# Kernel tuning notes

Hardware: AMD Instinct MI355X
Metric: run time of the kernel (lower is better)

Reference implementation:

```python
import jax, jax.numpy as jnp
import numpy as np

B, N, H, W = 4, 16, 480, 640
Hf, Wf, C = 120, 160, 128
NUM_CLASSES = 14
NUM_EXPERTS = NUM_CLASSES - 1  # 13 per-class ROI experts
ROI = 14  # ROI-align output resolution


def setup_inputs() -> dict:
    key = jax.random.key(0)
    ks = jax.random.split(key, 20)
    inp = {
        'depth': jax.random.normal(ks[0], (B, 1, H, W), jnp.float32),
        'context': jax.random.normal(ks[1], (B, 192, Hf, Wf), jnp.float32),
        'input_feature_map': jax.random.normal(ks[2], (B, C, Hf, Wf), jnp.float32),
        'bin_num': 64,
        'min_depth': 1,
        'max_depth': 10,
        'masks': jax.random.uniform(ks[3], (B, N, Hf, Wf), jnp.float32),
        'instances': jax.random.uniform(ks[4], (B, N, H, W), jnp.float32),
        'boxes': jax.random.uniform(ks[5], (B, N, 4), jnp.float32),
        'labels': jax.random.randint(ks[6], (B, N), 0, NUM_EXPERTS),
    }
    s = 0.05
    # per-class (expert) parameters, stacked on leading expert axis
    inp['w_conv_s'] = s * jax.random.normal(ks[7], (NUM_EXPERTS, C, C, 3, 3), jnp.float32)
    inp['b_conv_s'] = jnp.zeros((NUM_EXPERTS, C), jnp.float32)
    inp['w_fc'] = s * jax.random.normal(ks[8], (NUM_EXPERTS, 2, C), jnp.float32)
    inp['b_fc'] = jnp.zeros((NUM_EXPERTS, 2), jnp.float32)
    inp['w_conv_c1'] = s * jax.random.normal(ks[9], (NUM_EXPERTS, 64, C, 3, 3), jnp.float32)
    inp['b_conv_c1'] = jnp.zeros((NUM_EXPERTS, 64), jnp.float32)
    inp['w_conv_c2'] = s * jax.random.normal(ks[10], (NUM_EXPERTS, 1, 64, 3, 3), jnp.float32)
    inp['b_conv_c2'] = jnp.zeros((NUM_EXPERTS, 1), jnp.float32)
    return inp


def _boxes_norm(boxes_flat):
    # map raw rand [M,4] -> valid normalized (y1,x1,y2,x2) in [0,1]
    y1 = 0.6 * boxes_flat[:, 0]
    x1 = 0.6 * boxes_flat[:, 1]
    y2 = y1 + 0.1 + 0.3 * boxes_flat[:, 2]
    x2 = x1 + 0.1 + 0.3 * boxes_flat[:, 3]
    return y1, x1, y2, x2


def _roi_align(fmap, batch_idx, boxes_flat, R):
    # fmap [B,C,Hf,Wf] -> [M,C,R,R] bilinear ROI sampling (irregular gather)
    _, _, hf, wf = fmap.shape
    y1, x1, y2, x2 = _boxes_norm(boxes_flat)
    t = (jnp.arange(R, dtype=fmap.dtype) + 0.5) / R
    ys = (y1[:, None] + (y2 - y1)[:, None] * t) * (hf - 1)  # [M,R]
    xs = (x1[:, None] + (x2 - x1)[:, None] * t) * (wf - 1)
    y0 = jnp.clip(jnp.floor(ys).astype(jnp.int32), 0, hf - 2)
    x0 = jnp.clip(jnp.floor(xs).astype(jnp.int32), 0, wf - 2)
    wy = jnp.clip(ys - y0, 0.0, 1.0)[:, :, None, None]   # [M,R,1,1]
    wx = jnp.clip(xs - x0, 0.0, 1.0)[:, None, :, None]   # [M,1,R,1]
    b = batch_idx[:, None, None]
    Y0 = y0[:, :, None]
    X0 = x0[:, None, :]
    def g(dy, dx):
        return fmap[b, :, Y0 + dy, X0 + dx]  # [M,R,R,C]
    out = (g(0, 0) * (1 - wy) * (1 - wx) + g(0, 1) * (1 - wy) * wx
           + g(1, 0) * wy * (1 - wx) + g(1, 1) * wy * wx)
    return jnp.transpose(out, (0, 3, 1, 2))  # [M,C,R,R]


def _conv(x, w, b):
    # x [Cin,R,R], w [Cout,Cin,3,3] -> [Cout,R,R]
    y = jax.lax.conv_general_dilated(x[None], w, (1, 1), 'SAME',
                                     dimension_numbers=('NCHW', 'OIHW', 'NCHW'))[0]
    return y + b[:, None, None]

_conv_v = jax.vmap(_conv)  # per-instance expert conv (per-instance weights)


def reference(depth, context, input_feature_map, bin_num, min_depth, max_depth,
              masks, instances, boxes, labels,
              w_conv_s, b_conv_s, w_fc, b_fc, w_conv_c1, b_conv_c1, w_conv_c2, b_conv_c2):
    b_, n_, h, w = instances.shape
    M = b_ * n_
    lab = labels.reshape(M)
    batch_idx = jnp.repeat(jnp.arange(b_), n_)
    boxes_flat = boxes.reshape(M, 4)

    # shared ROI gather of class-routed instances
    roi = _roi_align(input_feature_map, batch_idx, boxes_flat, ROI)  # [M,C,R,R]

    # hard routing: gather each instance's class-expert weights by label
    hs = jax.nn.relu(_conv_v(roi, w_conv_s[lab], b_conv_s[lab]))     # [M,C,R,R]
    gap = hs.mean(axis=(2, 3))                                        # [M,C]
    ss = jnp.einsum('mc,moc->mo', gap, w_fc[lab]) + b_fc[lab]         # [M,2]
    scale = ss[:, 0].reshape(b_, n_)
    shift = ss[:, 1].reshape(b_, n_)

    h1 = jax.nn.relu(_conv_v(roi, w_conv_c1[lab], b_conv_c1[lab]))    # [M,64,R,R]
    c = _conv_v(h1, w_conv_c2[lab], b_conv_c2[lab])                   # [M,1,R,R]
    canonical = jax.image.resize(c, (M, 1, h, w), method='bilinear')
    canonical = canonical.reshape(b_, n_, h, w)

    # loss_type == 0: relu(.).clamp(min=0.001) == max(., 0.001)
    depth_r = jnp.maximum(canonical * scale[..., None, None] + shift[..., None, None], 0.001)
    return depth_r, canonical, scale, shift
```

## Files before the change

### kernel.cpp

```cpp
#include <hip/hip_runtime.h>


typedef unsigned short bfu;
typedef __attribute__((ext_vector_type(8))) short bf16x8;
typedef __attribute__((ext_vector_type(4))) float f32x4;

__device__ __forceinline__ float bf2f(bfu u) {
  union { unsigned int i; float f; } v;
  v.i = ((unsigned int)u) << 16;
  return v.f;
}
__device__ __forceinline__ bfu f2bf(float f) {
  union { float f; unsigned int i; } v;
  v.f = f;
  unsigned int u = v.i;
  u = (u + 0x7fffu + ((u >> 16) & 1u)) >> 16;
  return (bfu)u;
}

#define B_  4
#define N_  16
#define M_  64
#define H_  480
#define W_  640
#define HF  120
#define WF  160
#define C_  128
#define R_  14
#define PIX 196
#define NE  13
#define KK  1152

#define WS_XB    0
#define WS_XH    802816
#define WS_C     1204224
#define WS_GAP   1216768
#define WS_SCALE 1224960
#define WS_SHIFT 1225024
#define WS_WF    1225088
#define WS_BIASF 2662784
#define WS_W2    2665280
#define WS_B2    2672768
#define WS_WFC   2672784
#define WS_BFC   2676112

#define XB_BLOCKS 256
#define PREP_BLOCKS 1024

__global__ __launch_bounds__(256) void prep_xb_kernel(
    const float* __restrict__ fmap, const float* __restrict__ boxes,
    const float* __restrict__ w_s, const float* __restrict__ b_s,
    const float* __restrict__ w_fc, const float* __restrict__ b_fc,
    const float* __restrict__ w_c1, const float* __restrict__ b_c1,
    const float* __restrict__ w_c2, const float* __restrict__ b_c2,
    float* __restrict__ ws)
{
  int tid = threadIdx.x;
  if (blockIdx.x < XB_BLOCKS) {
    __shared__ int iy0[R_], ix0[R_];
    __shared__ float swy[R_], swx[R_];
    __shared__ unsigned int lt[PIX][17];
    int m  = blockIdx.x >> 2;
    int cb = (blockIdx.x & 3) * 32;
    if (tid < 2*R_) {
      int r = tid % R_;
      bool isY = tid < R_;
      float b0 = boxes[m*4 + (isY ? 0 : 1)];
      float b2 = boxes[m*4 + (isY ? 2 : 3)];
      float lo = 0.6f * b0;
      float hi = lo + 0.1f + 0.3f * b2;
      float t = ((float)r + 0.5f) / (float)R_;
      float dim = isY ? (float)(HF-1) : (float)(WF-1);
      float s = (lo + (hi - lo) * t) * dim;
      int maxi = isY ? (HF-2) : (WF-2);
      int i0 = (int)floorf(s);
      i0 = i0 < 0 ? 0 : (i0 > maxi ? maxi : i0);
      float w = s - (float)i0;
      w = w < 0.f ? 0.f : (w > 1.f ? 1.f : w);
      if (isY) { iy0[r] = i0; swy[r] = w; } else { ix0[r] = i0; swx[r] = w; }
    }
    __syncthreads();
    int bi = m / N_;
    const float* fb = fmap + ((size_t)bi * C_ + cb) * HF * WF;
    if (tid < PIX) {
      int ry = tid / 14, rx = tid - (tid/14)*14;
      int y0 = iy0[ry], x0 = ix0[rx];
      float wy = swy[ry], wx = swx[rx];
      float w00 = (1.f-wy)*(1.f-wx), w01 = (1.f-wy)*wx;
      float w10 = wy*(1.f-wx),       w11 = wy*wx;
      const float* fp = fb + (size_t)y0*WF + x0;
      #pragma unroll 4
      for (int c2 = 0; c2 < 16; ++c2) {
        const float* f0 = fp + (size_t)(2*c2)*HF*WF;
        const float* f1 = f0 + (size_t)HF*WF;
        float v0 = f0[0]*w00 + f0[1]*w01 + f0[WF]*w10 + f0[WF+1]*w11;
        float v1 = f1[0]*w00 + f1[1]*w01 + f1[WF]*w10 + f1[WF+1]*w11;
        lt[tid][c2] = (unsigned int)f2bf(v0) | ((unsigned int)f2bf(v1) << 16);
      }
    }
    __syncthreads();
    unsigned int* xbw = (unsigned int*)(ws + WS_XB);
    for (int idx = tid; idx < PIX*16; idx += 256) {
      int p = idx >> 4, c2 = idx & 15;
      xbw[((size_t)m*PIX + p)*64 + (cb >> 1) + c2] = lt[p][c2];
    }
    return;
  }

  const int P0 = NE*192*KK;
  const int P1 = NE*192;
  const int P2 = NE*576;
  const int P3 = NE;
  const int P4 = NE*256;
  const int P5 = NE*2;
  const int P6 = M_*C_;
  int total = P0+P1+P2+P3+P4+P5+P6;
  bfu* wf = (bfu*)(ws + WS_WF);
  for (int idx = (blockIdx.x - XB_BLOCKS)*256 + tid; idx < total;
       idx += PREP_BLOCKS*256) {
    int d = idx;
    if (d < P0) {
      int e = d / (192*KK);
      int r = d - e*(192*KK);
      int oc = r / KK;
      int k  = r - oc*KK;
      int kidx = k >> 7, ic = k & 127;
      float v = (oc < 128) ? w_s[((e*128 + oc)*128 + ic)*9 + kidx]
                           : w_c1[((e*64 + (oc-128))*128 + ic)*9 + kidx];
      wf[d] = f2bf(v);
      continue;
    }
    d -= P0;
    if (d < P1) {
      int e = d / 192, oc = d - e*192;
      ws[WS_BIASF + d] = (oc < 128) ? b_s[e*128 + oc] : b_c1[e*64 + oc - 128];
      continue;
    }
    d -= P1;
    if (d < P2) {
      int e = d / 576, k = d - e*576;
      int kidx = k >> 6, ic = k & 63;
      ws[WS_W2 + d] = w_c2[(e*64 + ic)*9 + kidx];
      continue;
    }
    d -= P2;
    if (d < P3) { ws[WS_B2 + d] = b_c2[d]; continue; }
    d -= P3;
    if (d < P4) { ws[WS_WFC + d] = w_fc[d]; continue; }
    d -= P4;
    if (d < P5) { ws[WS_BFC + d] = b_fc[d]; continue; }
    d -= P5;
    ws[WS_GAP + d] = 0.f;
  }
}

__global__ __launch_bounds__(256) void gemm_kernel(
    const int* __restrict__ labels, float* __restrict__ ws)
{
  __shared__ bfu lA[128*32];
  __shared__ bfu lB[128*32];
  const bfu* Xb = (const bfu*)(ws + WS_XB);
  const bfu* WFp = (const bfu*)(ws + WS_WF);
  const float* biasf = ws + WS_BIASF;
  float* gap = ws + WS_GAP;
  bfu* Xh = (bfu*)(ws + WS_XH);

  int bx = blockIdx.x;
  int m  = bx >> 2;
  int mb = (bx >> 1) & 1;
  int nb = bx & 1;
  int e = labels[m];
  int tid = threadIdx.x;
  int wave = tid >> 6, lane = tid & 63;
  int wm = wave >> 1, wn = wave & 1;
  int l15 = lane & 15, q = lane >> 4;

  int row0 = tid >> 2, row1 = row0 + 64;
  int kc = tid & 3;
  int loff0 = row0*32 + (kc ^ ((row0 >> 1) & 3))*8;
  int loff1 = row1*32 + (kc ^ ((row1 >> 1) & 3))*8;
  int g0 = mb*128 + row0, g1 = mb*128 + row1;
  bool av0 = g0 < 192, av1 = g1 < 192;
  const bfu* wfe = WFp + (size_t)e*192*KK;
  const bfu* wr0 = wfe + (size_t)g0*KK + kc*8;
  const bfu* wr1 = wfe + (size_t)g1*KK + kc*8;
  int pg0 = nb*128 + row0, pg1 = nb*128 + row1;
  int py0 = pg0 / 14, px0 = pg0 - (pg0/14)*14;
  int py1 = pg1 / 14, px1 = pg1 - (pg1/14)*14;
  bool pv0 = pg0 < PIX, pv1 = pg1 < PIX;
  const bfu* xbm = Xb + (size_t)m*PIX*128;

  f32x4 acc[4][4];
  #pragma unroll
  for (int i = 0; i < 4; ++i)
    #pragma unroll
    for (int j = 0; j < 4; ++j)
      acc[i][j] = (f32x4){0.f, 0.f, 0.f, 0.f};

  const uint4 z4 = make_uint4(0,0,0,0);
  uint4 na0, na1, nb0, nb1;
  auto issue = [&](int s, uint4& A0, uint4& A1, uint4& B0, uint4& B1) {
    int kidx = s >> 2, icc = s & 3;
    int t3 = kidx / 3;
    int dy = t3 - 1, dx = (kidx - t3*3) - 1;
    A0 = av0 ? *(const uint4*)(wr0 + s*32) : z4;
    A1 = av1 ? *(const uint4*)(wr1 + s*32) : z4;
    int ys0 = py0 + dy, xs0 = px0 + dx;
    int ys1 = py1 + dy, xs1 = px1 + dx;
    bool v0 = pv0 && (unsigned)ys0 < 14u && (unsigned)xs0 < 14u;
    bool v1 = pv1 && (unsigned)ys1 < 14u && (unsigned)xs1 < 14u;
    B0 = v0 ? *(const uint4*)(xbm + (size_t)(ys0*14+xs0)*128 + icc*32 + kc*8) : z4;
    B1 = v1 ? *(const uint4*)(xbm + (size_t)(ys1*14+xs1)*128 + icc*32 + kc*8) : z4;
  };
  issue(0, na0, na1, nb0, nb1);

  for (int s = 0; s < 36; ++s) {
    __syncthreads();
    *(uint4*)&lA[loff0] = na0;
    *(uint4*)&lA[loff1] = na1;
    *(uint4*)&lB[loff0] = nb0;
    *(uint4*)&lB[loff1] = nb1;
    __syncthreads();
    if (s < 35) issue(s+1, na0, na1, nb0, nb1);
    bf16x8 af[4], bfr[4];
    #pragma unroll
    for (int i = 0; i < 4; ++i) {
      int r = wm*64 + i*16 + l15;
      af[i] = *(const bf16x8*)&lA[r*32 + (q ^ ((r >> 1) & 3))*8];
    }
    #pragma unroll
    for (int j = 0; j < 4; ++j) {
      int r = wn*64 + j*16 + l15;
      bfr[j] = *(const bf16x8*)&lB[r*32 + (q ^ ((r >> 1) & 3))*8];
    }
    #pragma unroll
    for (int i = 0; i < 4; ++i)
      #pragma unroll
      for (int j = 0; j < 4; ++j)
        acc[i][j] = __builtin_amdgcn_mfma_f32_16x16x32_bf16(af[i], bfr[j], acc[i][j], 0, 0, 0);
  }

  if (mb == 0) {
    #pragma unroll
    for (int i = 0; i < 4; ++i) {
      int ocb = wm*64 + i*16 + q*4;
      f32x4 bv = *(const f32x4*)&biasf[e*192 + ocb];
      #pragma unroll
      for (int r = 0; r < 4; ++r) {
        float sum = 0.f;
        #pragma unroll
        for (int j = 0; j < 4; ++j) {
          int p = nb*128 + wn*64 + j*16 + l15;
          float v = acc[i][j][r] + bv[r];
          v = v > 0.f ? v : 0.f;
          if (p < PIX) sum += v;
        }
        sum += __shfl_xor(sum, 1);
        sum += __shfl_xor(sum, 2);
        sum += __shfl_xor(sum, 4);
        sum += __shfl_xor(sum, 8);
        if (l15 == 0) atomicAdd(&gap[m*C_ + ocb + r], sum);
      }
    }
  } else if (wm == 0) {
    #pragma unroll
    for (int i = 0; i < 4; ++i) {
      int icb = i*16 + q*4;
      f32x4 bv = *(const f32x4*)&biasf[e*192 + 128 + icb];
      #pragma unroll
      for (int j = 0; j < 4; ++j) {
        int p = nb*128 + wn*64 + j*16 + l15;
        if (p < PIX) {
          ushort4 pk;
          float v0 = acc[i][j][0] + bv[0]; v0 = v0 > 0.f ? v0 : 0.f;
          float v1 = acc[i][j][1] + bv[1]; v1 = v1 > 0.f ? v1 : 0.f;
          float v2 = acc[i][j][2] + bv[2]; v2 = v2 > 0.f ? v2 : 0.f;
          float v3 = acc[i][j][3] + bv[3]; v3 = v3 > 0.f ? v3 : 0.f;
          pk.x = f2bf(v0); pk.y = f2bf(v1); pk.z = f2bf(v2); pk.w = f2bf(v3);
          *(ushort4*)&Xh[((size_t)m*PIX + p)*64 + icb] = pk;
        }
      }
    }
  }
}

__global__ __launch_bounds__(256) void convc2_kernel(
    const int* __restrict__ labels, float* __restrict__ ws,
    float* __restrict__ out)
{
  __shared__ bfu xh[PIX*64];
  __shared__ float w2l[576];
  int m = blockIdx.x;
  int e = labels[m];
  int tid = threadIdx.x;
  int wave = tid >> 6, lane = tid & 63;

  if (wave < 2) {
    const float* g  = ws + WS_GAP + m*C_;
    const float* wv = ws + WS_WFC + (e*2 + wave)*C_;
    float s = g[lane]*wv[lane] + g[lane+64]*wv[lane+64];
    #pragma unroll
    for (int d = 32; d; d >>= 1) s += __shfl_xor(s, d);
    if (lane == 0) {
      s = ws[WS_BFC + e*2 + wave] + s * (1.f/(float)PIX);
      size_t base = (size_t)2 * M_ * H_ * W_;
      if (wave == 0) { ws[WS_SCALE + m] = s; out[base + m] = s; }
      else           { ws[WS_SHIFT + m] = s; out[base + M_ + m] = s; }
    }
  }

  const bfu* Xh = (const bfu*)(ws + WS_XH) + (size_t)m*PIX*64;
  for (int i = tid; i < PIX*64/8; i += 256)
    *(uint4*)&xh[i*8] = *(const uint4*)&Xh[i*8];
  for (int i = tid; i < 576; i += 256)
    w2l[i] = ws[WS_W2 + e*576 + i];
  __syncthreads();
  if (tid < PIX) {
    int y = tid / 14, x = tid - (tid/14)*14;
    float acc = 0.f;
    #pragma unroll
    for (int kidx = 0; kidx < 9; ++kidx) {
      int ys = y + kidx/3 - 1, xs = x + (kidx - (kidx/3)*3) - 1;
      if ((unsigned)ys < 14u && (unsigned)xs < 14u) {
        const bfu* xr = xh + (ys*14 + xs)*64;
        const float* wr = w2l + kidx*64;
        #pragma unroll
        for (int cc = 0; cc < 8; ++cc) {
          bf16x8 xv = *(const bf16x8*)&xr[cc*8];
          f32x4 wa = *(const f32x4*)&wr[cc*8];
          f32x4 wb = *(const f32x4*)&wr[cc*8 + 4];
          acc += bf2f((bfu)xv[0])*wa[0] + bf2f((bfu)xv[1])*wa[1]
               + bf2f((bfu)xv[2])*wa[2] + bf2f((bfu)xv[3])*wa[3]
               + bf2f((bfu)xv[4])*wb[0] + bf2f((bfu)xv[5])*wb[1]
               + bf2f((bfu)xv[6])*wb[2] + bf2f((bfu)xv[7])*wb[3];
        }
      }
    }
    ws[WS_C + m*PIX + tid] = acc + ws[WS_B2 + e];
  }
}

__global__ __launch_bounds__(256) void resize_kernel(
    const float* __restrict__ ws_c, const float* __restrict__ ws_scale,
    const float* __restrict__ ws_shift, float* __restrict__ out)
{
  __shared__ float cs[PIX];
  int bx = blockIdx.x;
  int m = bx / 150;
  int chunk = bx % 150;
  int tid = threadIdx.x;
  if (tid < PIX) cs[tid] = ws_c[m*PIX + tid];
  __syncthreads();
  float sc = ws_scale[m], sh = ws_shift[m];
  int q0 = chunk*2048 + tid*8;
  int y = q0 / W_;
  int x0i = q0 - y*W_;
  float py = ((float)y + 0.5f) * (14.f/(float)H_) - 0.5f;
  py = fminf(fmaxf(py, 0.f), 13.f);
  int y0 = (int)py; y0 = y0 > 12 ? 12 : y0;
  float wy = py - (float)y0;
  const float* r0 = cs + y0*R_;
  const float* r1 = r0 + R_;
  float vd[8], vc[8];
  #pragma unroll
  for (int u = 0; u < 8; ++u) {
    int x = x0i + u;
    float px = ((float)x + 0.5f) * (14.f/(float)W_) - 0.5f;
    px = fminf(fmaxf(px, 0.f), 13.f);
    int xq = (int)px; xq = xq > 12 ? 12 : xq;
    float wx = px - (float)xq;
    float v = (r0[xq]*(1.f-wx) + r0[xq+1]*wx) * (1.f-wy)
            + (r1[xq]*(1.f-wx) + r1[xq+1]*wx) * wy;
    vc[u] = v;
    vd[u] = fmaxf(v*sc + sh, 0.001f);
  }
  size_t base = (size_t)m * H_ * W_ + q0;
  float* od = out + base;
  float* oc = out + (size_t)M_*H_*W_ + base;
  f32x4 d0 = (f32x4){vd[0], vd[1], vd[2], vd[3]};
  f32x4 d1 = (f32x4){vd[4], vd[5], vd[6], vd[7]};
  f32x4 c0 = (f32x4){vc[0], vc[1], vc[2], vc[3]};
  f32x4 c1 = (f32x4){vc[4], vc[5], vc[6], vc[7]};
  __builtin_nontemporal_store(d0, (f32x4*)(od));
  __builtin_nontemporal_store(d1, (f32x4*)(od + 4));
  __builtin_nontemporal_store(c0, (f32x4*)(oc));
  __builtin_nontemporal_store(c1, (f32x4*)(oc + 4));
}

extern "C" void kernel_launch(void* const* d_in, const int* in_sizes, int n_in,
                              void* d_out, int out_size, void* d_ws, size_t ws_size,
                              hipStream_t stream) {
  const float* fmap  = (const float*)d_in[2];
  const float* boxes = (const float*)d_in[8];
  const int* labels  = (const int*)d_in[9];
  const float* w_s  = (const float*)d_in[10];
  const float* b_s  = (const float*)d_in[11];
  const float* w_fc = (const float*)d_in[12];
  const float* b_fc = (const float*)d_in[13];
  const float* w_c1 = (const float*)d_in[14];
  const float* b_c1 = (const float*)d_in[15];
  const float* w_c2 = (const float*)d_in[16];
  const float* b_c2 = (const float*)d_in[17];
  float* ws = (float*)d_ws;
  float* out = (float*)d_out;

  hipLaunchKernelGGL(prep_xb_kernel, dim3(XB_BLOCKS + PREP_BLOCKS), dim3(256), 0, stream,
                     fmap, boxes, w_s, b_s, w_fc, b_fc, w_c1, b_c1, w_c2, b_c2, ws);
  hipLaunchKernelGGL(gemm_kernel, dim3(M_*4), dim3(256), 0, stream,
                     labels, ws);
  hipLaunchKernelGGL(convc2_kernel, dim3(M_), dim3(256), 0, stream,
                     labels, ws, out);
  hipLaunchKernelGGL(resize_kernel, dim3(M_*150), dim3(256), 0, stream,
                     ws + WS_C, ws + WS_SCALE, ws + WS_SHIFT, out);
}
```

Baseline: 376.2 us.

## Fuse conv_c2 and FC head into GEMM kernel with full-pixel tiles

The GEMM kernel now covers all 196 pixels per block (2 blocks per instance instead of 4), so the GAP reduction and the 64-channel hidden activation stay entirely within one block. The FC scale/shift head and the conv_c2 3x3 convolution then run in that block using shared memory, which removes the separate convc2 kernel launch, the global Xh round trip, and the GAP atomics along with their zeroing. In exchange there are fewer blocks (128), more accumulator registers per thread (26 MFMA tiles), and the conv_c2 tail runs serially after the GEMM inside the block.

```diff
diff --git a/kernel.cpp b/kernel.cpp
--- a/kernel.cpp
+++ b/kernel.cpp
@@ -32,9 +32,7 @@
 #define KK  1152
 
 #define WS_XB    0
-#define WS_XH    802816
 #define WS_C     1204224
-#define WS_GAP   1216768
 #define WS_SCALE 1224960
 #define WS_SHIFT 1225024
 #define WS_WF    1225088
@@ -113,8 +111,7 @@
   const int P3 = NE;
   const int P4 = NE*256;
   const int P5 = NE*2;
-  const int P6 = M_*C_;
-  int total = P0+P1+P2+P3+P4+P5+P6;
+  int total = P0+P1+P2+P3+P4+P5;
   bfu* wf = (bfu*)(ws + WS_WF);
   for (int idx = (blockIdx.x - XB_BLOCKS)*256 + tid; idx < total;
        idx += PREP_BLOCKS*256) {
@@ -148,110 +145,114 @@
     d -= P3;
     if (d < P4) { ws[WS_WFC + d] = w_fc[d]; continue; }
     d -= P4;
-    if (d < P5) { ws[WS_BFC + d] = b_fc[d]; continue; }
-    d -= P5;
-    ws[WS_GAP + d] = 0.f;
+    if (d < P5) { ws[WS_BFC + d] = b_fc[d]; }
   }
 }
 
 __global__ __launch_bounds__(256) void gemm_kernel(
-    const int* __restrict__ labels, float* __restrict__ ws)
+    const int* __restrict__ labels, float* __restrict__ ws,
+    float* __restrict__ out)
 {
-  __shared__ bfu lA[128*32];
-  __shared__ bfu lB[128*32];
-  const bfu* Xb = (const bfu*)(ws + WS_XB);
+  __shared__ __align__(16) char smem[28672];
+  bfu* lA = (bfu*)smem;
+  bfu* lB = (bfu*)(smem + 8192);
+
+  const bfu* Xb  = (const bfu*)(ws + WS_XB);
   const bfu* WFp = (const bfu*)(ws + WS_WF);
   const float* biasf = ws + WS_BIASF;
-  float* gap = ws + WS_GAP;
-  bfu* Xh = (bfu*)(ws + WS_XH);
 
   int bx = blockIdx.x;
-  int m  = bx >> 2;
-  int mb = (bx >> 1) & 1;
-  int nb = bx & 1;
+  int m  = bx >> 1;
+  int mb = bx & 1;
   int e = labels[m];
   int tid = threadIdx.x;
   int wave = tid >> 6, lane = tid & 63;
-  int wm = wave >> 1, wn = wave & 1;
   int l15 = lane & 15, q = lane >> 4;
 
-  int row0 = tid >> 2, row1 = row0 + 64;
+  int arow0 = tid >> 2, arow1 = arow0 + 64;
   int kc = tid & 3;
-  int loff0 = row0*32 + (kc ^ ((row0 >> 1) & 3))*8;
-  int loff1 = row1*32 + (kc ^ ((row1 >> 1) & 3))*8;
-  int g0 = mb*128 + row0, g1 = mb*128 + row1;
+  int aoff0 = arow0*32 + (kc ^ ((arow0 >> 1) & 3))*8;
+  int aoff1 = arow1*32 + (kc ^ ((arow1 >> 1) & 3))*8;
+  int g0 = mb*128 + arow0, g1 = mb*128 + arow1;
   bool av0 = g0 < 192, av1 = g1 < 192;
   const bfu* wfe = WFp + (size_t)e*192*KK;
   const bfu* wr0 = wfe + (size_t)g0*KK + kc*8;
   const bfu* wr1 = wfe + (size_t)g1*KK + kc*8;
-  int pg0 = nb*128 + row0, pg1 = nb*128 + row1;
-  int py0 = pg0 / 14, px0 = pg0 - (pg0/14)*14;
-  int py1 = pg1 / 14, px1 = pg1 - (pg1/14)*14;
-  bool pv0 = pg0 < PIX, pv1 = pg1 < PIX;
+
+  int bpy[4], bpx[4], boff[4];
+  bool bu[4], bva[4];
+  #pragma unroll
+  for (int k2 = 0; k2 < 4; ++k2) {
+    int u = tid + 256*k2;
+    int r = u >> 2;
+    bu[k2]  = (u < 832);
+    bva[k2] = bu[k2] && (r < PIX);
+    int py = r / 14;
+    bpy[k2] = py; bpx[k2] = r - py*14;
+    boff[k2] = r*32 + (kc ^ ((r >> 1) & 3))*8;
+  }
   const bfu* xbm = Xb + (size_t)m*PIX*128;
 
-  f32x4 acc[4][4];
+  f32x4 acc[2][13];
   #pragma unroll
-  for (int i = 0; i < 4; ++i)
+  for (int i = 0; i < 2; ++i)
     #pragma unroll
-    for (int j = 0; j < 4; ++j)
+    for (int j = 0; j < 13; ++j)
       acc[i][j] = (f32x4){0.f, 0.f, 0.f, 0.f};
 
   const uint4 z4 = make_uint4(0,0,0,0);
-  uint4 na0, na1, nb0, nb1;
-  auto issue = [&](int s, uint4& A0, uint4& A1, uint4& B0, uint4& B1) {
+  uint4 pa0, pa1, pb[4];
+  auto issue = [&](int s) {
     int kidx = s >> 2, icc = s & 3;
     int t3 = kidx / 3;
     int dy = t3 - 1, dx = (kidx - t3*3) - 1;
-    A0 = av0 ? *(const uint4*)(wr0 + s*32) : z4;
-    A1 = av1 ? *(const uint4*)(wr1 + s*32) : z4;
-    int ys0 = py0 + dy, xs0 = px0 + dx;
-    int ys1 = py1 + dy, xs1 = px1 + dx;
-    bool v0 = pv0 && (unsigned)ys0 < 14u && (unsigned)xs0 < 14u;
-    bool v1 = pv1 && (unsigned)ys1 < 14u && (unsigned)xs1 < 14u;
-    B0 = v0 ? *(const uint4*)(xbm + (size_t)(ys0*14+xs0)*128 + icc*32 + kc*8) : z4;
-    B1 = v1 ? *(const uint4*)(xbm + (size_t)(ys1*14+xs1)*128 + icc*32 + kc*8) : z4;
+    pa0 = av0 ? *(const uint4*)(wr0 + s*32) : z4;
+    pa1 = av1 ? *(const uint4*)(wr1 + s*32) : z4;
+    #pragma unroll
+    for (int k2 = 0; k2 < 4; ++k2) {
+      int ys = bpy[k2] + dy, xs = bpx[k2] + dx;
+      bool v = bva[k2] && (unsigned)ys < 14u && (unsigned)xs < 14u;
+      pb[k2] = v ? *(const uint4*)(xbm + (size_t)(ys*14+xs)*128 + icc*32 + kc*8) : z4;
+    }
   };
-  issue(0, na0, na1, nb0, nb1);
+  issue(0);
 
   for (int s = 0; s < 36; ++s) {
     __syncthreads();
-    *(uint4*)&lA[loff0] = na0;
-    *(uint4*)&lA[loff1] = na1;
-    *(uint4*)&lB[loff0] = nb0;
-    *(uint4*)&lB[loff1] = nb1;
-    __syncthreads();
-    if (s < 35) issue(s+1, na0, na1, nb0, nb1);
-    bf16x8 af[4], bfr[4];
+    *(uint4*)&lA[aoff0] = pa0;
+    *(uint4*)&lA[aoff1] = pa1;
     #pragma unroll
-    for (int i = 0; i < 4; ++i) {
-      int r = wm*64 + i*16 + l15;
-      af[i] = *(const bf16x8*)&lA[r*32 + (q ^ ((r >> 1) & 3))*8];
-    }
+    for (int k2 = 0; k2 < 4; ++k2)
+      if (bu[k2]) *(uint4*)&lB[boff[k2]] = pb[k2];
+    __syncthreads();
+    if (s < 35) issue(s+1);
+    int ra0 = wave*32 + l15, ra1 = ra0 + 16;
+    bf16x8 af0 = *(const bf16x8*)&lA[ra0*32 + (q ^ ((ra0 >> 1) & 3))*8];
+    bf16x8 af1 = *(const bf16x8*)&lA[ra1*32 + (q ^ ((ra1 >> 1) & 3))*8];
     #pragma unroll
-    for (int j = 0; j < 4; ++j) {
-      int r = wn*64 + j*16 + l15;
-      bfr[j] = *(const bf16x8*)&lB[r*32 + (q ^ ((r >> 1) & 3))*8];
-    }
+    for (int j = 0; j < 13; ++j) {
+      int rb = j*16 + l15;
+      bf16x8 bfv = *(const bf16x8*)&lB[rb*32 + (q ^ ((rb >> 1) & 3))*8];
+      acc[0][j] = __builtin_amdgcn_mfma_f32_16x16x32_bf16(af0, bfv, acc[0][j], 0, 0, 0);
+      acc[1][j] = __builtin_amdgcn_mfma_f32_16x16x32_bf16(af1, bfv, acc[1][j], 0, 0, 0);
+    }
+  }
+
+  __syncthreads();
+
+  if (mb == 0) {
+    float* gapL = (float*)(smem + 25088);
     #pragma unroll
-    for (int i = 0; i < 4; ++i)
-      #pragma unroll
-      for (int j = 0; j < 4; ++j)
-        acc[i][j] = __builtin_amdgcn_mfma_f32_16x16x32_bf16(af[i], bfr[j], acc[i][j], 0, 0, 0);
-  }
-
-  if (mb == 0) {
-    #pragma unroll
-    for (int i = 0; i < 4; ++i) {
-      int ocb = wm*64 + i*16 + q*4;
-      f32x4 bv = *(const f32x4*)&biasf[e*192 + ocb];
+    for (int i = 0; i < 2; ++i) {
+      int ocb = wave*32 + i*16 + q*4;
+      f32x4 bv4 = *(const f32x4*)&biasf[e*192 + ocb];
       #pragma unroll
       for (int r = 0; r < 4; ++r) {
         float sum = 0.f;
         #pragma unroll
-        for (int j = 0; j < 4; ++j) {
-          int p = nb*128 + wn*64 + j*16 + l15;
-          float v = acc[i][j][r] + bv[r];
+        for (int j = 0; j < 13; ++j) {
+          int p = j*16 + l15;
+          float v = acc[i][j][r] + bv4[r];
           v = v > 0.f ? v : 0.f;
           if (p < PIX) sum += v;
         }
@@ -259,84 +260,71 @@
         sum += __shfl_xor(sum, 2);
         sum += __shfl_xor(sum, 4);
         sum += __shfl_xor(sum, 8);
-        if (l15 == 0) atomicAdd(&gap[m*C_ + ocb + r], sum);
+        if (l15 == 0) gapL[ocb + r] = sum;
       }
     }
-  } else if (wm == 0) {
-    #pragma unroll
-    for (int i = 0; i < 4; ++i) {
-      int icb = i*16 + q*4;
-      f32x4 bv = *(const f32x4*)&biasf[e*192 + 128 + icb];
+    __syncthreads();
+    if (wave < 2) {
+      const float* wv = ws + WS_WFC + (e*2 + wave)*C_;
+      float s = gapL[lane]*wv[lane] + gapL[lane+64]*wv[lane+64];
       #pragma unroll
-      for (int j = 0; j < 4; ++j) {
-        int p = nb*128 + wn*64 + j*16 + l15;
-        if (p < PIX) {
-          ushort4 pk;
-          float v0 = acc[i][j][0] + bv[0]; v0 = v0 > 0.f ? v0 : 0.f;
-          float v1 = acc[i][j][1] + bv[1]; v1 = v1 > 0.f ? v1 : 0.f;
-          float v2 = acc[i][j][2] + bv[2]; v2 = v2 > 0.f ? v2 : 0.f;
-          float v3 = acc[i][j][3] + bv[3]; v3 = v3 > 0.f ? v3 : 0.f;
-          pk.x = f2bf(v0); pk.y = f2bf(v1); pk.z = f2bf(v2); pk.w = f2bf(v3);
-          *(ushort4*)&Xh[((size_t)m*PIX + p)*64 + icb] = pk;
+      for (int d = 32; d; d >>= 1) s += __shfl_xor(s, d);
+      if (lane == 0) {
+        s = ws[WS_BFC + e*2 + wave] + s * (1.f/(float)PIX);
+        size_t base = (size_t)2 * M_ * H_ * W_;
+        if (wave == 0) { ws[WS_SCALE + m] = s; out[base + m] = s; }
+        else           { ws[WS_SHIFT + m] = s; out[base + M_ + m] = s; }
+      }
+    }
+  } else {
+    bfu* xh = (bfu*)smem;
+    float* w2l = (float*)(smem + 25088);
+    for (int i2 = tid; i2 < 576; i2 += 256)
+      w2l[i2] = ws[WS_W2 + e*576 + i2];
+    if (wave < 2) {
+      #pragma unroll
+      for (int i = 0; i < 2; ++i) {
+        int icb = wave*32 + i*16 + q*4;
+        f32x4 bv4 = *(const f32x4*)&biasf[e*192 + 128 + icb];
+        #pragma unroll
+        for (int j = 0; j < 13; ++j) {
+          int p = j*16 + l15;
+          if (p < PIX) {
+            ushort4 pk;
+            float v0 = acc[i][j][0] + bv4[0]; v0 = v0 > 0.f ? v0 : 0.f;
+            float v1 = acc[i][j][1] + bv4[1]; v1 = v1 > 0.f ? v1 : 0.f;
+            float v2 = acc[i][j][2] + bv4[2]; v2 = v2 > 0.f ? v2 : 0.f;
+            float v3 = acc[i][j][3] + bv4[3]; v3 = v3 > 0.f ? v3 : 0.f;
+            pk.x = f2bf(v0); pk.y = f2bf(v1); pk.z = f2bf(v2); pk.w = f2bf(v3);
+            *(ushort4*)&xh[p*64 + icb] = pk;
+          }
         }
       }
     }
-  }
-}
-
-__global__ __launch_bounds__(256) void convc2_kernel(
-    const int* __restrict__ labels, float* __restrict__ ws,
-    float* __restrict__ out)
-{
-  __shared__ bfu xh[PIX*64];
-  __shared__ float w2l[576];
-  int m = blockIdx.x;
-  int e = labels[m];
-  int tid = threadIdx.x;
-  int wave = tid >> 6, lane = tid & 63;
-
-  if (wave < 2) {
-    const float* g  = ws + WS_GAP + m*C_;
-    const float* wv = ws + WS_WFC + (e*2 + wave)*C_;
-    float s = g[lane]*wv[lane] + g[lane+64]*wv[lane+64];
-    #pragma unroll
-    for (int d = 32; d; d >>= 1) s += __shfl_xor(s, d);
-    if (lane == 0) {
-      s = ws[WS_BFC + e*2 + wave] + s * (1.f/(float)PIX);
-      size_t base = (size_t)2 * M_ * H_ * W_;
-      if (wave == 0) { ws[WS_SCALE + m] = s; out[base + m] = s; }
-      else           { ws[WS_SHIFT + m] = s; out[base + M_ + m] = s; }
-    }
-  }
-
-  const bfu* Xh = (const bfu*)(ws + WS_XH) + (size_t)m*PIX*64;
-  for (int i = tid; i < PIX*64/8; i += 256)
-    *(uint4*)&xh[i*8] = *(const uint4*)&Xh[i*8];
-  for (int i = tid; i < 576; i += 256)
-    w2l[i] = ws[WS_W2 + e*576 + i];
-  __syncthreads();
-  if (tid < PIX) {
-    int y = tid / 14, x = tid - (tid/14)*14;
-    float acc = 0.f;
-    #pragma unroll
-    for (int kidx = 0; kidx < 9; ++kidx) {
-      int ys = y + kidx/3 - 1, xs = x + (kidx - (kidx/3)*3) - 1;
-      if ((unsigned)ys < 14u && (unsigned)xs < 14u) {
-        const bfu* xr = xh + (ys*14 + xs)*64;
-        const float* wr = w2l + kidx*64;
-        #pragma unroll
-        for (int cc = 0; cc < 8; ++cc) {
-          bf16x8 xv = *(const bf16x8*)&xr[cc*8];
-          f32x4 wa = *(const f32x4*)&wr[cc*8];
-          f32x4 wb = *(const f32x4*)&wr[cc*8 + 4];
-          acc += bf2f((bfu)xv[0])*wa[0] + bf2f((bfu)xv[1])*wa[1]
-               + bf2f((bfu)xv[2])*wa[2] + bf2f((bfu)xv[3])*wa[3]
-               + bf2f((bfu)xv[4])*wb[0] + bf2f((bfu)xv[5])*wb[1]
-               + bf2f((bfu)xv[6])*wb[2] + bf2f((bfu)xv[7])*wb[3];
+    __syncthreads();
+    if (tid < PIX) {
+      int y = tid / 14, x = tid - (tid/14)*14;
+      float cacc = 0.f;
+      #pragma unroll
+      for (int kidx = 0; kidx < 9; ++kidx) {
+        int ys = y + kidx/3 - 1, xs = x + (kidx - (kidx/3)*3) - 1;
+        if ((unsigned)ys < 14u && (unsigned)xs < 14u) {
+          const bfu* xr = xh + (ys*14 + xs)*64;
+          const float* wr = w2l + kidx*64;
+          #pragma unroll
+          for (int cc = 0; cc < 8; ++cc) {
+            bf16x8 xv = *(const bf16x8*)&xr[cc*8];
+            f32x4 wa = *(const f32x4*)&wr[cc*8];
+            f32x4 wb = *(const f32x4*)&wr[cc*8 + 4];
+            cacc += bf2f((bfu)xv[0])*wa[0] + bf2f((bfu)xv[1])*wa[1]
+                  + bf2f((bfu)xv[2])*wa[2] + bf2f((bfu)xv[3])*wa[3]
+                  + bf2f((bfu)xv[4])*wb[0] + bf2f((bfu)xv[5])*wb[1]
+                  + bf2f((bfu)xv[6])*wb[2] + bf2f((bfu)xv[7])*wb[3];
+          }
         }
       }
-    }
-    ws[WS_C + m*PIX + tid] = acc + ws[WS_B2 + e];
+      ws[WS_C + m*PIX + tid] = cacc + ws[WS_B2 + e];
+    }
   }
 }
 
@@ -406,9 +394,7 @@
 
   hipLaunchKernelGGL(prep_xb_kernel, dim3(XB_BLOCKS + PREP_BLOCKS), dim3(256), 0, stream,
                      fmap, boxes, w_s, b_s, w_fc, b_fc, w_c1, b_c1, w_c2, b_c2, ws);
-  hipLaunchKernelGGL(gemm_kernel, dim3(M_*4), dim3(256), 0, stream,
-                     labels, ws);
-  hipLaunchKernelGGL(convc2_kernel, dim3(M_), dim3(256), 0, stream,
+  hipLaunchKernelGGL(gemm_kernel, dim3(M_*2), dim3(256), 0, stream,
                      labels, ws, out);
   hipLaunchKernelGGL(resize_kernel, dim3(M_*150), dim3(256), 0, stream,
                      ws + WS_C, ws + WS_SCALE, ws + WS_SHIFT, out);
```

Result: slower. 419.0 us (+11.4%).

## Fuse conv_c2 and scale/shift computation into resize kernel per output chunk

Applied to the files above, without the earlier changes.

The small conv_c2 kernel, which ran on only 64 blocks, is merged into the resize kernel. Each of the 9600 resize blocks now loads the few feature rows its output chunk needs (up to 5 rows), recomputes the 14-wide conv rows it samples, and recomputes scale and shift. This removes one launch and the serial low-occupancy stage along with its workspace round trip. The cost is redundant conv and reduction work repeated across chunks plus extra global loads per block.

```diff
diff --git a/kernel.cpp b/kernel.cpp
--- a/kernel.cpp
+++ b/kernel.cpp
@@ -33,10 +33,7 @@
 
 #define WS_XB    0
 #define WS_XH    802816
-#define WS_C     1204224
 #define WS_GAP   1216768
-#define WS_SCALE 1224960
-#define WS_SHIFT 1225024
 #define WS_WF    1225088
 #define WS_BIASF 2662784
 #define WS_W2    2665280
@@ -284,16 +281,44 @@
   }
 }
 
-__global__ __launch_bounds__(256) void convc2_kernel(
-    const int* __restrict__ labels, float* __restrict__ ws,
+__global__ __launch_bounds__(256) void resize_kernel(
+    const int* __restrict__ labels, const float* __restrict__ ws,
     float* __restrict__ out)
 {
-  __shared__ bfu xh[PIX*64];
+  __shared__ bfu xh[5*14*64];
   __shared__ float w2l[576];
-  int m = blockIdx.x;
+  __shared__ float cs[3*14];
+  __shared__ float ssh[2];
+  int bx = blockIdx.x;
+  int m = bx / 150;
+  int chunk = bx - m*150;
   int e = labels[m];
   int tid = threadIdx.x;
   int wave = tid >> 6, lane = tid & 63;
+
+  auto srcy = [](int y)->float {
+    float py = ((float)y + 0.5f) * (14.f/(float)H_) - 0.5f;
+    return fminf(fmaxf(py, 0.f), 13.f);
+  };
+  int q0 = chunk*2048;
+  int yo0 = q0 / W_;
+  int yo1 = (q0 + 2047) / W_;
+  int Y0 = (int)srcy(yo0); Y0 = Y0 > 12 ? 12 : Y0;
+  int Yb = (int)srcy(yo1); Yb = Yb > 12 ? 12 : Yb;
+  int XR0 = Y0 - 1;
+
+  const bfu* XhG = (const bfu*)(ws + WS_XH) + (size_t)m*PIX*64;
+  const uint4 z4 = make_uint4(0,0,0,0);
+  for (int i = tid; i < 560; i += 256) {
+    int slot = i / 112, rem = i - slot*112;
+    int r = XR0 + slot;
+    uint4 v = z4;
+    if ((unsigned)r < 14u)
+      v = *(const uint4*)(XhG + (size_t)r*896 + rem*8);
+    *(uint4*)&xh[slot*896 + rem*8] = v;
+  }
+  for (int i = tid; i < 576; i += 256)
+    w2l[i] = ws[WS_W2 + e*576 + i];
 
   if (wave < 2) {
     const float* g  = ws + WS_GAP + m*C_;
@@ -303,64 +328,52 @@
     for (int d = 32; d; d >>= 1) s += __shfl_xor(s, d);
     if (lane == 0) {
       s = ws[WS_BFC + e*2 + wave] + s * (1.f/(float)PIX);
-      size_t base = (size_t)2 * M_ * H_ * W_;
-      if (wave == 0) { ws[WS_SCALE + m] = s; out[base + m] = s; }
-      else           { ws[WS_SHIFT + m] = s; out[base + M_ + m] = s; }
-    }
-  }
-
-  const bfu* Xh = (const bfu*)(ws + WS_XH) + (size_t)m*PIX*64;
-  for (int i = tid; i < PIX*64/8; i += 256)
-    *(uint4*)&xh[i*8] = *(const uint4*)&Xh[i*8];
-  for (int i = tid; i < 576; i += 256)
-    w2l[i] = ws[WS_W2 + e*576 + i];
+      ssh[wave] = s;
+      if (chunk == 0) {
+        size_t base = (size_t)2 * M_ * H_ * W_;
+        out[base + wave*M_ + m] = s;
+      }
+    }
+  }
   __syncthreads();
-  if (tid < PIX) {
-    int y = tid / 14, x = tid - (tid/14)*14;
-    float acc = 0.f;
-    #pragma unroll
-    for (int kidx = 0; kidx < 9; ++kidx) {
-      int ys = y + kidx/3 - 1, xs = x + (kidx - (kidx/3)*3) - 1;
-      if ((unsigned)ys < 14u && (unsigned)xs < 14u) {
-        const bfu* xr = xh + (ys*14 + xs)*64;
-        const float* wr = w2l + kidx*64;
-        #pragma unroll
-        for (int cc = 0; cc < 8; ++cc) {
-          bf16x8 xv = *(const bf16x8*)&xr[cc*8];
-          f32x4 wa = *(const f32x4*)&wr[cc*8];
-          f32x4 wb = *(const f32x4*)&wr[cc*8 + 4];
-          acc += bf2f((bfu)xv[0])*wa[0] + bf2f((bfu)xv[1])*wa[1]
-               + bf2f((bfu)xv[2])*wa[2] + bf2f((bfu)xv[3])*wa[3]
-               + bf2f((bfu)xv[4])*wb[0] + bf2f((bfu)xv[5])*wb[1]
-               + bf2f((bfu)xv[6])*wb[2] + bf2f((bfu)xv[7])*wb[3];
+
+  if (tid < 42) {
+    int rr = tid / 14, x = tid - rr*14;
+    int ys = Y0 + rr;
+    if (ys <= 13) {
+      float cacc = 0.f;
+      #pragma unroll
+      for (int kidx = 0; kidx < 9; ++kidx) {
+        int ysrc = ys + kidx/3 - 1, xsrc = x + (kidx - (kidx/3)*3) - 1;
+        if ((unsigned)ysrc < 14u && (unsigned)xsrc < 14u) {
+          const bfu* xr = xh + ((ysrc - XR0)*14 + xsrc)*64;
+          const float* wr = w2l + kidx*64;
+          #pragma unroll
+          for (int cc = 0; cc < 8; ++cc) {
+            bf16x8 xv = *(const bf16x8*)&xr[cc*8];
+            f32x4 wa = *(const f32x4*)&wr[cc*8];
+            f32x4 wb = *(const f32x4*)&wr[cc*8 + 4];
+            cacc += bf2f((bfu)xv[0])*wa[0] + bf2f((bfu)xv[1])*wa[1]
+                  + bf2f((bfu)xv[2])*wa[2] + bf2f((bfu)xv[3])*wa[3]
+                  + bf2f((bfu)xv[4])*wb[0] + bf2f((bfu)xv[5])*wb[1]
+                  + bf2f((bfu)xv[6])*wb[2] + bf2f((bfu)xv[7])*wb[3];
+          }
         }
       }
-    }
-    ws[WS_C + m*PIX + tid] = acc + ws[WS_B2 + e];
-  }
-}
-
-__global__ __launch_bounds__(256) void resize_kernel(
-    const float* __restrict__ ws_c, const float* __restrict__ ws_scale,
-    const float* __restrict__ ws_shift, float* __restrict__ out)
-{
-  __shared__ float cs[PIX];
-  int bx = blockIdx.x;
-  int m = bx / 150;
-  int chunk = bx % 150;
-  int tid = threadIdx.x;
-  if (tid < PIX) cs[tid] = ws_c[m*PIX + tid];
+      cs[tid] = cacc + ws[WS_B2 + e];
+    }
+  }
   __syncthreads();
-  float sc = ws_scale[m], sh = ws_shift[m];
-  int q0 = chunk*2048 + tid*8;
-  int y = q0 / W_;
-  int x0i = q0 - y*W_;
-  float py = ((float)y + 0.5f) * (14.f/(float)H_) - 0.5f;
-  py = fminf(fmaxf(py, 0.f), 13.f);
+
+  float sc = ssh[0], sh = ssh[1];
+  int qt = q0 + tid*8;
+  int y = qt / W_;
+  int x0i = qt - y*W_;
+  float py = srcy(y);
   int y0 = (int)py; y0 = y0 > 12 ? 12 : y0;
   float wy = py - (float)y0;
-  const float* r0 = cs + y0*R_;
-  const float* r1 = r0 + R_;
+  const float* r0 = cs + (y0 - Y0)*14;
+  const float* r1 = r0 + 14;
   float vd[8], vc[8];
   #pragma unroll
   for (int u = 0; u < 8; ++u) {
@@ -374,7 +387,7 @@
     vc[u] = v;
     vd[u] = fmaxf(v*sc + sh, 0.001f);
   }
-  size_t base = (size_t)m * H_ * W_ + q0;
+  size_t base = (size_t)m * H_ * W_ + qt;
   float* od = out + base;
   float* oc = out + (size_t)M_*H_*W_ + base;
   f32x4 d0 = (f32x4){vd[0], vd[1], vd[2], vd[3]};
@@ -408,8 +421,6 @@
                      fmap, boxes, w_s, b_s, w_fc, b_fc, w_c1, b_c1, w_c2, b_c2, ws);
   hipLaunchKernelGGL(gemm_kernel, dim3(M_*4), dim3(256), 0, stream,
                      labels, ws);
-  hipLaunchKernelGGL(convc2_kernel, dim3(M_), dim3(256), 0, stream,
+  hipLaunchKernelGGL(resize_kernel, dim3(M_*150), dim3(256), 0, stream,
                      labels, ws, out);
-  hipLaunchKernelGGL(resize_kernel, dim3(M_*150), dim3(256), 0, stream,
-                     ws + WS_C, ws + WS_SCALE, ws + WS_SHIFT, out);
-}
+}
```

Measured after the change: 382.4 us. About the same (+1.6%).
